# Kernel optimization log

Measured on AMD Instinct MI355X. Metric: run time of the kernel, lower is better.

The kernel has to match this reference:

```python
import jax, jax.numpy as jnp
import numpy as np

EPS_L2 = 1e-12  # torch F.normalize eps
EPS_NORM = 1e-5  # ZeroCenteredRMSNorm eps


def _linear(x, W, b):
    return x @ W.T + b


def _silu(x):
    return x * jax.nn.sigmoid(x)


def _l2norm(x):
    n = jnp.sqrt(jnp.sum(x * x, axis=-1, keepdims=True))
    return x / jnp.maximum(n, EPS_L2)


def _dwconv_causal(x, w, b):
    # x: [B,S,d]; w: [d,1,4] (torch depthwise conv weight); causal pad 3 left
    y = jax.lax.conv_general_dilated(
        x.transpose(0, 2, 1), w, window_strides=(1,), padding=[(3, 0)],
        dimension_numbers=('NCH', 'OIH', 'NCH'), feature_group_count=w.shape[0])
    return y.transpose(0, 2, 1) + b


def _zc_rmsnorm(x, weight):
    xm = x - jnp.mean(x, axis=-1, keepdims=True)
    var = jnp.mean(xm * xm, axis=-1, keepdims=True)
    return xm * jax.lax.rsqrt(var + EPS_NORM) * weight


def _gated_delta_core(q, k, v, alpha, beta):
    # q,k,v: [B,S,d]; alpha,beta: [B,S]
    B, S, d = q.shape
    S0 = jnp.zeros((B, d, d), dtype=q.dtype)

    def step(St, inp):
        qt, kt, vt, at, bt = inp  # [B,d],[B,d],[B,d],[B],[B]
        # S @ (a*(I - b k k^T)) = a*(S - b*(S k) k^T)   (rank-1 update, same math)
        Sk = jnp.einsum('bij,bj->bi', St, kt)            # [B,d]
        a = at[:, None, None]
        b = bt[:, None, None]
        Sn = a * (St - b * Sk[:, :, None] * kt[:, None, :]) + b * vt[:, :, None] * kt[:, None, :]
        ot = jnp.einsum('bij,bj->bi', Sn, qt)            # [B,d]
        return Sn, ot

    xs = (q.transpose(1, 0, 2), k.transpose(1, 0, 2), v.transpose(1, 0, 2),
          alpha.T, beta.T)
    _, outs = jax.lax.scan(step, S0, xs)  # outs: [S,B,d]
    return outs.transpose(1, 0, 2)


def setup_inputs() -> dict:
    key = jax.random.key(0)
    ks = jax.random.split(key, 16)
    B, S, d = 8, 2048, 512
    w = lambda k, shape: (jax.random.normal(k, shape, jnp.float32) * 0.02)
    return {
        'x': jax.random.normal(ks[0], (B, S, d), jnp.float32),
        'Wq': w(ks[1], (d, d)), 'bq': jnp.zeros((d,), jnp.float32),
        'Wk': w(ks[2], (d, d)), 'bk': jnp.zeros((d,), jnp.float32),
        'Wv': w(ks[3], (d, d)), 'bv': jnp.zeros((d,), jnp.float32),
        'Wa': w(ks[4], (1, d)), 'ba': jnp.zeros((1,), jnp.float32),
        'Wb': w(ks[5], (1, d)), 'bb': jnp.zeros((1,), jnp.float32),
        'cwq': w(ks[6], (d, 1, 4)), 'cbq': jnp.zeros((d,), jnp.float32),
        'cwk': w(ks[7], (d, 1, 4)), 'cbk': jnp.zeros((d,), jnp.float32),
        'cwv': w(ks[8], (d, 1, 4)), 'cbv': jnp.zeros((d,), jnp.float32),
        'norm_w': jnp.ones((d,), jnp.float32),
        'Wg': w(ks[9], (d, d)), 'bg': jnp.zeros((d,), jnp.float32),
        'Wo': w(ks[10], (d, d)), 'bo': jnp.zeros((d,), jnp.float32),
    }


def reference(x, Wq, bq, Wk, bk, Wv, bv, Wa, ba, Wb, bb,
              cwq, cbq, cwk, cbk, cwv, cbv, norm_w, Wg, bg, Wo, bo):
    q_c = _dwconv_causal(_linear(x, Wq, bq), cwq, cbq)
    k_c = _dwconv_causal(_linear(x, Wk, bk), cwk, cbk)
    v_c = _dwconv_causal(_linear(x, Wv, bv), cwv, cbv)
    q = _l2norm(_silu(q_c))
    k = _l2norm(_silu(k_c))
    v = _silu(v_c)
    alpha = jax.nn.sigmoid(_linear(x, Wa, ba))[..., 0]  # [B,S]
    beta = jax.nn.sigmoid(_linear(x, Wb, bb))[..., 0]   # [B,S]
    gdn = _gated_delta_core(q, k, v, alpha, beta)       # [B,S,d]
    gdn = _zc_rmsnorm(gdn, norm_w)
    gate = _silu(_linear(x, Wg, bg))
    return _linear(gdn * gate, Wo, bo)
```

## Files before the change

kernel.cpp:

```cpp
#include <hip/hip_runtime.h>
#include <math.h>

typedef unsigned short u16;
typedef unsigned int u32;
typedef short short8 __attribute__((ext_vector_type(8)));
typedef float f32x4 __attribute__((ext_vector_type(4)));

#define B_ 8
#define S_ 2048
#define D_ 512
#define N_ (B_ * S_)
#define ND_ ((size_t)N_ * D_)
#define CC_ 32
#define NC_ (S_ / CC_)
#define SV_ 16
#define TB_ 8

__device__ __forceinline__ u16 f2bf(float f) {
  union { float f; u32 i; } v; v.f = f;
  u32 i = v.i;
  i += 0x7FFFu + ((i >> 16) & 1u);
  return (u16)(i >> 16);
}
__device__ __forceinline__ float bf2f(u16 u) {
  union { u32 i; float f; } v; v.i = ((u32)u) << 16; return v.f;
}
__device__ __forceinline__ float sigm(float x) { return 1.0f / (1.0f + expf(-x)); }

__device__ __forceinline__ void glds16(const u16* g, u16* l) {
  __builtin_amdgcn_global_load_lds(
      (const __attribute__((address_space(1))) void*)g,
      (__attribute__((address_space(3))) void*)l, 16, 0, 0);
}

__global__ __launch_bounds__(256) void cvt_bf16(const float* __restrict__ s,
                                                u16* __restrict__ d, int n)
{
  const int i = (blockIdx.x * 256 + threadIdx.x) * 4;
  if (i < n) {
    const float4 v = *(const float4*)(s + i);
    ushort4 o;
    o.x = f2bf(v.x); o.y = f2bf(v.y); o.z = f2bf(v.z); o.w = f2bf(v.w);
    *(ushort4*)(d + i) = o;
  }
}

__global__ __launch_bounds__(256) void cvt_w5(
    const float* __restrict__ w0, const float* __restrict__ w1,
    const float* __restrict__ w2, const float* __restrict__ w3,
    const float* __restrict__ w4, u16* __restrict__ d)
{
  const int z = blockIdx.y;
  const float* s = (z == 0) ? w0 : (z == 1) ? w1 : (z == 2) ? w2 : (z == 3) ? w3 : w4;
  u16* o = d + (size_t)z * 512 * 512;
  const int i = (blockIdx.x * 256 + threadIdx.x) * 4;
  const float4 v = *(const float4*)(s + i);
  ushort4 t;
  t.x = f2bf(v.x); t.y = f2bf(v.y); t.z = f2bf(v.z); t.w = f2bf(v.w);
  *(ushort4*)(o + i) = t;
}

__device__ __forceinline__ void gemm_body(
    const u16* __restrict__ A, const u16* __restrict__ W,
    const float* __restrict__ bias, float* __restrict__ out,
    int m0, int n0, u16* As, u16* Bs)
{
  const int tid = threadIdx.x;
  const int lane = tid & 63, wave = tid >> 6;
  const int wm = (wave >> 1) * 64, wn = (wave & 1) * 64;
  const int l15 = lane & 15, quad = lane >> 4;

  const int lr = tid >> 2;
  const int ks = (tid & 3) ^ ((tid >> 3) & 3);
  u16* abase0 = As + wave * 512;
  u16* abase1 = As + 2048 + wave * 512;
  u16* bbase0 = Bs + wave * 512;
  u16* bbase1 = Bs + 2048 + wave * 512;

  f32x4 acc[4][4];
#pragma unroll
  for (int i = 0; i < 4; i++)
#pragma unroll
    for (int j = 0; j < 4; j++) acc[i][j] = (f32x4){0.f, 0.f, 0.f, 0.f};

  for (int k0 = 0; k0 < 512; k0 += 32) {
    __syncthreads();
    glds16(A + (size_t)(m0 + lr) * 512 + k0 + ks * 8, abase0);
    glds16(A + (size_t)(m0 + 64 + lr) * 512 + k0 + ks * 8, abase1);
    glds16(W + (size_t)(n0 + lr) * 512 + k0 + ks * 8, bbase0);
    glds16(W + (size_t)(n0 + 64 + lr) * 512 + k0 + ks * 8, bbase1);
    __syncthreads();
    short8 af[4], bf[4];
#pragma unroll
    for (int mt = 0; mt < 4; mt++) {
      const int row = wm + mt * 16 + l15;
      af[mt] = *(const short8*)(As + row * 32 + ((quad ^ ((row >> 1) & 3)) * 8));
    }
#pragma unroll
    for (int nt = 0; nt < 4; nt++) {
      const int row = wn + nt * 16 + l15;
      bf[nt] = *(const short8*)(Bs + row * 32 + ((quad ^ ((row >> 1) & 3)) * 8));
    }
#pragma unroll
    for (int mt = 0; mt < 4; mt++)
#pragma unroll
      for (int nt = 0; nt < 4; nt++)
        acc[mt][nt] = __builtin_amdgcn_mfma_f32_16x16x32_bf16(af[mt], bf[nt], acc[mt][nt], 0, 0, 0);
  }
#pragma unroll
  for (int mt = 0; mt < 4; mt++) {
#pragma unroll
    for (int nt = 0; nt < 4; nt++) {
      const int col = n0 + wn + nt * 16 + l15;
      const float bcol = bias[col];
#pragma unroll
      for (int r = 0; r < 4; r++) {
        const int row = m0 + wm + mt * 16 + quad * 4 + r;
        out[(size_t)row * 512 + col] = acc[mt][nt][r] + bcol;
      }
    }
  }
}

__global__ __launch_bounds__(256) void gemm_bt(
    const u16* __restrict__ A, const u16* __restrict__ W,
    const float* __restrict__ bias, float* __restrict__ out)
{
  __shared__ u16 As[128 * 32];
  __shared__ u16 Bs[128 * 32];
  gemm_body(A, W, bias, out, blockIdx.x * 128, blockIdx.y * 128, As, Bs);
}

__global__ __launch_bounds__(256) void gemm_bt4(
    const u16* __restrict__ A, const u16* __restrict__ Wbase,
    const float* __restrict__ b0, const float* __restrict__ b1,
    const float* __restrict__ b2, const float* __restrict__ b3,
    float* __restrict__ outbase)
{
  __shared__ u16 As[128 * 32];
  __shared__ u16 Bs[128 * 32];
  const int z = blockIdx.z;
  const u16* W = Wbase + (size_t)z * 512 * 512;
  const float* bias = (z == 0) ? b0 : (z == 1) ? b1 : (z == 2) ? b2 : b3;
  float* out = outbase + (size_t)z * ND_;
  gemm_body(A, W, bias, out, blockIdx.x * 128, blockIdx.y * 128, As, Bs);
}

__global__ __launch_bounds__(256) void ab_kernel(
    const float* __restrict__ x, const float* __restrict__ Wa, const float* __restrict__ ba,
    const float* __restrict__ Wb, const float* __restrict__ bb,
    float* __restrict__ alpha, float* __restrict__ beta)
{
  const int lane = threadIdx.x & 63, wave = threadIdx.x >> 6;
  const int row = blockIdx.x * 4 + wave;
  const float4 x0 = *(const float4*)(x + (size_t)row * 512 + lane * 8);
  const float4 x1 = *(const float4*)(x + (size_t)row * 512 + lane * 8 + 4);
  const float4 a0 = *(const float4*)(Wa + lane * 8);
  const float4 a1 = *(const float4*)(Wa + lane * 8 + 4);
  const float4 b0 = *(const float4*)(Wb + lane * 8);
  const float4 b1 = *(const float4*)(Wb + lane * 8 + 4);
  float da = x0.x*a0.x + x0.y*a0.y + x0.z*a0.z + x0.w*a0.w
           + x1.x*a1.x + x1.y*a1.y + x1.z*a1.z + x1.w*a1.w;
  float db = x0.x*b0.x + x0.y*b0.y + x0.z*b0.z + x0.w*b0.w
           + x1.x*b1.x + x1.y*b1.y + x1.z*b1.z + x1.w*b1.w;
#pragma unroll
  for (int m = 32; m >= 1; m >>= 1) { da += __shfl_xor(da, m, 64); db += __shfl_xor(db, m, 64); }
  if (lane == 0) {
    alpha[row] = sigm(da + ba[0]);
    beta[row]  = sigm(db + bb[0]);
  }
}

__global__ __launch_bounds__(256) void conv_act(
    const float* __restrict__ lq, const float* __restrict__ lk, const float* __restrict__ lv,
    const float* __restrict__ cwq, const float* __restrict__ cbq,
    const float* __restrict__ cwk, const float* __restrict__ cbk,
    const float* __restrict__ cwv, const float* __restrict__ cbv,
    u16* __restrict__ oq, u16* __restrict__ ok, float* __restrict__ ov)
{
  __shared__ float red[TB_][4];
  const int z = blockIdx.y;
  const int r0 = blockIdx.x * TB_;
  const int b = r0 / S_, t0 = r0 - b * S_;
  const float* lin = (z == 0) ? lq : (z == 1) ? lk : lv;
  const float* cw = (z == 0) ? cwq : (z == 1) ? cwk : cwv;
  const float* cb = (z == 0) ? cbq : (z == 1) ? cbk : cbv;
  const int tid = threadIdx.x;
  const int lane = tid & 63, wave = tid >> 6;

  float w4[2][4], bias[2];
#pragma unroll
  for (int e = 0; e < 2; e++) {
    const int ch = tid + e * 256;
    bias[e] = cb[ch];
#pragma unroll
    for (int tau = 0; tau < 4; tau++) w4[e][tau] = cw[ch * 4 + tau];
  }
  float win[2][TB_ + 3];
#pragma unroll
  for (int i = 0; i < TB_ + 3; i++) {
    const int tt = t0 - 3 + i;
#pragma unroll
    for (int e = 0; e < 2; e++)
      win[e][i] = (tt >= 0) ? lin[(size_t)(b * S_ + tt) * D_ + tid + e * 256] : 0.f;
  }
  float sv[2][TB_], ssq[TB_];
#pragma unroll
  for (int j = 0; j < TB_; j++) {
    float ss = 0.f;
#pragma unroll
    for (int e = 0; e < 2; e++) {
      float acc = bias[e];
#pragma unroll
      for (int tau = 0; tau < 4; tau++) acc = fmaf(win[e][j + tau], w4[e][tau], acc);
      const float s = acc * sigm(acc);
      sv[e][j] = s; ss = fmaf(s, s, ss);
    }
    ssq[j] = ss;
  }
  if (z < 2) {
#pragma unroll
    for (int j = 0; j < TB_; j++) {
#pragma unroll
      for (int m = 32; m >= 1; m >>= 1) ssq[j] += __shfl_xor(ssq[j], m, 64);
    }
    if (lane == 0) {
#pragma unroll
      for (int j = 0; j < TB_; j++) red[j][wave] = ssq[j];
    }
    __syncthreads();
    u16* outp = (z == 0) ? oq : ok;
#pragma unroll
    for (int j = 0; j < TB_; j++) {
      const float tot = red[j][0] + red[j][1] + red[j][2] + red[j][3];
      const float scale = 1.0f / fmaxf(sqrtf(tot), 1e-12f);
      outp[(size_t)(r0 + j) * D_ + tid] = f2bf(sv[0][j] * scale);
      outp[(size_t)(r0 + j) * D_ + tid + 256] = f2bf(sv[1][j] * scale);
    }
  } else {
#pragma unroll
    for (int j = 0; j < TB_; j++) {
      ov[(size_t)(r0 + j) * D_ + tid] = sv[0][j];
      ov[(size_t)(r0 + j) * D_ + tid + 256] = sv[1][j];
    }
  }
}

__global__ __launch_bounds__(256) void transpose_k(
    const u16* __restrict__ kh, u16* __restrict__ khT)
{
  __shared__ u16 T[64][68];
  const int b = blockIdx.z;
  const int t0 = blockIdx.x * 64;
  const int c0 = blockIdx.y * 64;
  const int tid = threadIdx.x;
  const int tr = tid >> 4;
  const int c4 = (tid & 15) * 4;
#pragma unroll
  for (int i = 0; i < 4; i++) {
    const int t = tr + i * 16;
    ushort4 v = *(const ushort4*)(kh + ((size_t)(b * S_ + t0 + t)) * 512 + c0 + c4);
    T[c4 + 0][t] = v.x; T[c4 + 1][t] = v.y; T[c4 + 2][t] = v.z; T[c4 + 3][t] = v.w;
  }
  __syncthreads();
#pragma unroll
  for (int i = 0; i < 4; i++) {
    const int ch = tr + i * 16;
    ushort4 v = *(const ushort4*)&T[ch][c4];
    *(ushort4*)(khT + ((size_t)(b * 512 + c0 + ch)) * S_ + t0 + c4) = v;
  }
}

__global__ __launch_bounds__(256) void prepass(
    const u16* __restrict__ kh, const u16* __restrict__ qh,
    float* __restrict__ vbU,
    const float* __restrict__ alpha, const float* __restrict__ beta,
    u16* __restrict__ Ag, float* __restrict__ gg, u16* __restrict__ Wc)
{
  __shared__ float KK[32][33];
  __shared__ float QK[32][33];
  __shared__ float Ml[32][33];
  __shared__ float Xs[32][33];
  __shared__ u16 Xb[32 * 40];
  __shared__ u16 VT[512 * 40];
  __shared__ float lg[32], cum[32], bet[32], gams[32];
  const int bc = blockIdx.x;
  const int b = bc >> 6, c = bc & 63;
  const int t0 = c * CC_;
  const int tid = threadIdx.x, lane = tid & 63, w = tid >> 6;
  const int l15 = lane & 15, quad = lane >> 4;
  const size_t rb = (size_t)b * S_ + t0;

  if (tid < 32) { lg[tid] = logf(alpha[b * S_ + t0 + tid]); bet[tid] = beta[b * S_ + t0 + tid]; }
  __syncthreads();
  if (tid < 32) {
    float s = 0.f;
    for (int u = 0; u <= tid; u++) s += lg[u];
    cum[tid] = s;
    gams[tid] = expf(s);
  }
  const int mi = w >> 1, ni = w & 1;
  f32x4 ck = (f32x4){0.f,0.f,0.f,0.f}, cq = ck;
#pragma unroll
  for (int kt = 0; kt < 16; kt++) {
    const int kc = kt * 32 + quad * 8;
    short8 afk = *(const short8*)(kh + (rb + mi * 16 + l15) * 512 + kc);
    short8 afq = *(const short8*)(qh + (rb + mi * 16 + l15) * 512 + kc);
    short8 bk  = *(const short8*)(kh + (rb + ni * 16 + l15) * 512 + kc);
    ck = __builtin_amdgcn_mfma_f32_16x16x32_bf16(afk, bk, ck, 0, 0, 0);
    cq = __builtin_amdgcn_mfma_f32_16x16x32_bf16(afq, bk, cq, 0, 0, 0);
  }
#pragma unroll
  for (int r = 0; r < 4; r++) {
    KK[mi * 16 + quad * 4 + r][ni * 16 + l15] = ck[r];
    QK[mi * 16 + quad * 4 + r][ni * 16 + l15] = cq[r];
  }
  __syncthreads();
  if (tid < 32) {
    gg[(size_t)bc * 64 + tid] = gams[tid];
    gg[(size_t)bc * 64 + 32 + tid] = expf(cum[31] - cum[tid]);
  }
#pragma unroll
  for (int rep = 0; rep < 4; rep++) {
    const int e = tid + rep * 256;
    const int t = e >> 5, s = e & 31;
    const float er = expf(cum[t] - cum[s]);
    Ml[t][s] = (s < t) ? bet[t] * er * KK[t][s] : 0.f;
    Ag[(size_t)bc * 1024 + t * 32 + s] = (s <= t) ? f2bf(QK[t][s] * er) : (u16)0;
  }
#pragma unroll
  for (int rep = 0; rep < 8; rep++) {
    const int e = tid + rep * 256;
    const int v = e & 511, so = e >> 9;
    short8 pk;
#pragma unroll
    for (int j = 0; j < 8; j++) {
      const int s = so * 8 + j;
      pk[j] = (short)f2bf(bet[s] * vbU[(rb + s) * 512 + v]);
    }
    *(short8*)&VT[v * 40 + so * 8] = pk;
  }
  __syncthreads();
  if (w == 0 && lane < 32) {
    const int j = lane;
    Xs[0][j] = (j == 0) ? 1.f : 0.f;
    for (int t = 1; t < 32; t++) {
      float a = (t == j) ? 1.f : 0.f;
      for (int u = 0; u < t; u++) a = fmaf(-Ml[t][u], Xs[u][j], a);
      Xs[t][j] = a;
    }
  }
  __syncthreads();
#pragma unroll
  for (int rep = 0; rep < 4; rep++) {
    const int e = tid + rep * 256;
    const int t = e >> 5, s = e & 31;
    Xb[t * 40 + s] = f2bf(Xs[t][s]);
  }
  __syncthreads();
  short8 xa[2];
  xa[0] = *(const short8*)&Xb[l15 * 40 + quad * 8];
  xa[1] = *(const short8*)&Xb[(16 + l15) * 40 + quad * 8];
#pragma unroll
  for (int ntr = 0; ntr < 8; ntr++) {
    const int nt = w * 8 + ntr;
    short8 bv = *(const short8*)&VT[(nt * 16 + l15) * 40 + quad * 8];
#pragma unroll
    for (int mt = 0; mt < 2; mt++) {
      f32x4 g = (f32x4){0.f, 0.f, 0.f, 0.f};
      g = __builtin_amdgcn_mfma_f32_16x16x32_bf16(xa[mt], bv, g, 0, 0, 0);
#pragma unroll
      for (int r = 0; r < 4; r++)
        vbU[(rb + mt * 16 + quad * 4 + r) * 512 + nt * 16 + l15] = g[r];
    }
  }
  __syncthreads();
#pragma unroll
  for (int rep = 0; rep < 8; rep++) {
    const int e = tid + rep * 256;
    const int v = e & 511, so = e >> 9;
    short8 pk;
#pragma unroll
    for (int j = 0; j < 8; j++) {
      const int s = so * 8 + j;
      pk[j] = (short)f2bf(bet[s] * gams[s] * bf2f(kh[(rb + s) * 512 + v]));
    }
    *(short8*)&VT[v * 40 + so * 8] = pk;
  }
  __syncthreads();
#pragma unroll
  for (int ntr = 0; ntr < 8; ntr++) {
    const int nt = w * 8 + ntr;
    short8 bv = *(const short8*)&VT[(nt * 16 + l15) * 40 + quad * 8];
#pragma unroll
    for (int mt = 0; mt < 2; mt++) {
      f32x4 g = (f32x4){0.f, 0.f, 0.f, 0.f};
      g = __builtin_amdgcn_mfma_f32_16x16x32_bf16(xa[mt], bv, g, 0, 0, 0);
#pragma unroll
      for (int r = 0; r < 4; r++)
        Wc[(size_t)bc * 16384 + (mt * 16 + quad * 4 + r) * 512 + nt * 16 + l15] = f2bf(g[r]);
    }
  }
}

__global__ __launch_bounds__(512) void scan_chunk(
    const u16* __restrict__ qh, const u16* __restrict__ khT,
    const u16* __restrict__ Wc, const float* __restrict__ U,
    const u16* __restrict__ Ag, const float* __restrict__ gg,
    float* __restrict__ gdn)
{
  __shared__ u16 S_A[16 * 520];
  __shared__ float P[2][2][32][16];
  __shared__ u16 Ct_T[16 * 40];
  __shared__ u16 Cr_T[16 * 40];
  __shared__ float OB[32][17];
  __shared__ float gam[32], grc[32];
  const int b = blockIdx.y;
  const int iv0 = blockIdx.x * SV_;
  const int tid = threadIdx.x, lane = tid & 63, w = tid >> 6;
  const int l15 = lane & 15, quad = lane >> 4;
  const int ttile = w & 1, mat = (w >> 1) & 1, khalf = w >> 2;
  const size_t bS = (size_t)b * S_;
  const int ct = tid >> 4, cv = tid & 15;

  f32x4 acc[4];
#pragma unroll
  for (int mt = 0; mt < 4; mt++) acc[mt] = (f32x4){0.f, 0.f, 0.f, 0.f};

  short8 nbf[8], ntk[4], nagf = {};
  float nUv = 0.f, ngam = 0.f, ngrc = 0.f;

#define SCAN_LOAD(CN) do {                                                          \
    const int t0n_ = (CN) * CC_;                                                    \
    const int bcn_ = b * 64 + (CN);                                                 \
    const u16* bsrc_ = mat ? (qh + (bS + t0n_ + ttile * 16 + l15) * 512 + khalf * 256) \
                           : (Wc + ((size_t)bcn_ * 32 + ttile * 16 + l15) * 512 + khalf * 256); \
    _Pragma("unroll")                                                               \
    for (int kt_ = 0; kt_ < 8; kt_++)                                               \
      nbf[kt_] = *(const short8*)(bsrc_ + kt_ * 32 + quad * 8);                     \
    _Pragma("unroll")                                                               \
    for (int mt_ = 0; mt_ < 4; mt_++)                                               \
      ntk[mt_] = *(const short8*)(khT + ((size_t)(b * 512 + w * 64 + mt_ * 16 + l15)) * S_ + t0n_ + quad * 8); \
    nUv = U[(bS + t0n_ + ct) * 512 + iv0 + cv];                                     \
    if (w < 2) nagf = *(const short8*)(Ag + (size_t)bcn_ * 1024 + (w * 16 + l15) * 32 + quad * 8); \
    if (tid < 32) { ngam = gg[(size_t)bcn_ * 64 + tid]; ngrc = gg[(size_t)bcn_ * 64 + 32 + tid]; } \
  } while (0)

  SCAN_LOAD(0);

#pragma unroll 1
  for (int c = 0; c < NC_; c++) {
    const int t0 = c * CC_;
    short8 bfrag[8], tk[4], agf;
#pragma unroll
    for (int kt = 0; kt < 8; kt++) bfrag[kt] = nbf[kt];
#pragma unroll
    for (int mt = 0; mt < 4; mt++) tk[mt] = ntk[mt];
    agf = nagf;
    const float Uv = nUv, gamv = ngam, grcv = ngrc;
    const int cn = (c + 1 < NC_) ? c + 1 : c;
    SCAN_LOAD(cn);
    if (tid < 32) { gam[tid] = gamv; grc[tid] = grcv; }
#pragma unroll
    for (int mt = 0; mt < 4; mt++) {
      ushort4 p;
      p.x = f2bf(acc[mt][0]); p.y = f2bf(acc[mt][1]);
      p.z = f2bf(acc[mt][2]); p.w = f2bf(acc[mt][3]);
      *(ushort4*)&S_A[l15 * 520 + w * 64 + mt * 16 + quad * 4] = p;
    }
    __syncthreads();
    f32x4 g = (f32x4){0.f, 0.f, 0.f, 0.f};
#pragma unroll
    for (int kt = 0; kt < 8; kt++) {
      short8 af = *(const short8*)&S_A[l15 * 520 + khalf * 256 + kt * 32 + quad * 8];
      g = __builtin_amdgcn_mfma_f32_16x16x32_bf16(af, bfrag[kt], g, 0, 0, 0);
    }
    *(f32x4*)&P[mat][khalf][ttile * 16 + l15][quad * 4] = g;
    __syncthreads();
    const float gCs = gam[31];
    {
      const float T1 = P[0][0][ct][cv] + P[0][1][ct][cv];
      const float T2 = P[1][0][ct][cv] + P[1][1][ct][cv];
      const float ctv = Uv - T1;
      Ct_T[cv * 40 + ct] = f2bf(ctv);
      Cr_T[cv * 40 + ct] = f2bf(ctv * grc[ct]);
      OB[ct][cv] = gam[ct] * T2;
    }
    __syncthreads();
    short8 bcf = *(const short8*)&Cr_T[l15 * 40 + quad * 8];
#pragma unroll
    for (int mt = 0; mt < 4; mt++) {
      acc[mt] = acc[mt] * gCs;
      acc[mt] = __builtin_amdgcn_mfma_f32_16x16x32_bf16(tk[mt], bcf, acc[mt], 0, 0, 0);
    }
    if (w < 2) {
      short8 ctf = *(const short8*)&Ct_T[l15 * 40 + quad * 8];
      f32x4 oo;
#pragma unroll
      for (int r = 0; r < 4; r++) oo[r] = OB[w * 16 + quad * 4 + r][l15];
      oo = __builtin_amdgcn_mfma_f32_16x16x32_bf16(agf, ctf, oo, 0, 0, 0);
#pragma unroll
      for (int r = 0; r < 4; r++)
        gdn[(bS + t0 + w * 16 + quad * 4 + r) * 512 + iv0 + l15] = oo[r];
    }
  }
#undef SCAN_LOAD
}

__global__ __launch_bounds__(256) void norm_gate(
    const float* __restrict__ gdn, const float* __restrict__ lg,
    const float* __restrict__ nw, u16* __restrict__ h)
{
  __shared__ float red[8];
  const int row = blockIdx.x, tid = threadIdx.x;
  const size_t base = (size_t)row * D_;
  const float g0 = gdn[base + tid], g1 = gdn[base + tid + 256];
  float sm = g0 + g1;
#pragma unroll
  for (int m = 32; m >= 1; m >>= 1) sm += __shfl_xor(sm, m, 64);
  if ((tid & 63) == 0) red[tid >> 6] = sm;
  __syncthreads();
  const float mean = (red[0] + red[1] + red[2] + red[3]) * (1.0f / 512.0f);
  const float x0 = g0 - mean, x1 = g1 - mean;
  float sq = x0 * x0 + x1 * x1;
#pragma unroll
  for (int m = 32; m >= 1; m >>= 1) sq += __shfl_xor(sq, m, 64);
  if ((tid & 63) == 0) red[4 + (tid >> 6)] = sq;
  __syncthreads();
  const float var = (red[4] + red[5] + red[6] + red[7]) * (1.0f / 512.0f);
  const float rst = rsqrtf(var + 1e-5f);
  const float gl0 = lg[base + tid];
  h[base + tid] = f2bf(x0 * rst * nw[tid] * (gl0 * sigm(gl0)));
  const float gl1 = lg[base + tid + 256];
  h[base + tid + 256] = f2bf(x1 * rst * nw[tid + 256] * (gl1 * sigm(gl1)));
}

extern "C" void kernel_launch(void* const* d_in, const int* in_sizes, int n_in,
                              void* d_out, int out_size, void* d_ws, size_t ws_size,
                              hipStream_t stream)
{
  const float* x   = (const float*)d_in[0];
  const float* Wq  = (const float*)d_in[1];
  const float* bq  = (const float*)d_in[2];
  const float* Wk  = (const float*)d_in[3];
  const float* bk  = (const float*)d_in[4];
  const float* Wv  = (const float*)d_in[5];
  const float* bv  = (const float*)d_in[6];
  const float* Wa  = (const float*)d_in[7];
  const float* ba  = (const float*)d_in[8];
  const float* Wb  = (const float*)d_in[9];
  const float* bb  = (const float*)d_in[10];
  const float* cwq = (const float*)d_in[11];
  const float* cbq = (const float*)d_in[12];
  const float* cwk = (const float*)d_in[13];
  const float* cbk = (const float*)d_in[14];
  const float* cwv = (const float*)d_in[15];
  const float* cbv = (const float*)d_in[16];
  const float* nw  = (const float*)d_in[17];
  const float* Wg  = (const float*)d_in[18];
  const float* bg  = (const float*)d_in[19];
  const float* Wo  = (const float*)d_in[20];
  const float* bo  = (const float*)d_in[21];

  float* ws    = (float*)d_ws;
  float* lin_q = ws;
  float* lin_k = ws + ND_;
  float* lin_v = ws + 2 * ND_;
  float* lin_g = ws + 3 * ND_;
  float* vb    = ws + 4 * ND_;
  u16*   qh    = (u16*)(ws + 5 * ND_);
  u16*   kh    = qh + ND_;
  float* alpha = ws + 6 * ND_;
  float* beta  = alpha + N_;
  u16*   xb    = (u16*)(beta + N_);
  u16*   wq_b  = xb + ND_;
  u16*   wk_b  = wq_b + 512 * 512;
  u16*   wv_b  = wk_b + 512 * 512;
  u16*   wg_b  = wv_b + 512 * 512;
  u16*   wo_b  = wg_b + 512 * 512;

  u16*   khT   = (u16*)lin_k;
  u16*   Agb   = khT + ND_;
  float* ggb   = (float*)(Agb + (size_t)512 * 1024);
  u16*   Wcb   = (u16*)lin_v;
  float* gdn   = lin_q;
  u16*   h     = (u16*)lin_v;

  const int NW = 512 * 512;
  cvt_bf16<<<(int)(ND_ / 1024), 256, 0, stream>>>(x, xb, (int)ND_);
  cvt_w5<<<dim3(NW / 1024, 5), 256, 0, stream>>>(Wq, Wk, Wv, Wg, Wo, wq_b);

  gemm_bt4<<<dim3(128, 4, 4), 256, 0, stream>>>(xb, wq_b, bq, bk, bv, bg, ws);
  ab_kernel<<<N_ / 4, 256, 0, stream>>>(x, Wa, ba, Wb, bb, alpha, beta);
  conv_act<<<dim3(N_ / TB_, 3), 256, 0, stream>>>(lin_q, lin_k, lin_v,
                                                  cwq, cbq, cwk, cbk, cwv, cbv, qh, kh, vb);
  transpose_k<<<dim3(S_ / 64, D_ / 64, B_), 256, 0, stream>>>(kh, khT);
  prepass<<<B_ * NC_, 256, 0, stream>>>(kh, qh, vb, alpha, beta, Agb, ggb, Wcb);
  scan_chunk<<<dim3(D_ / SV_, B_), 512, 0, stream>>>(qh, khT, Wcb, vb, Agb, ggb, gdn);
  norm_gate<<<N_, 256, 0, stream>>>(gdn, lin_g, nw, h);
  gemm_bt<<<dim3(128, 4), 256, 0, stream>>>(h, wo_b, bo, (float*)d_out);
}
```

Baseline: 477.7 us.

## Double chunk size to 64 in chunked delta-rule prepass and scan

Raises the chunk length of the chunked gated-delta scan from 32 to 64, which halves the number of sequential chunk iterations in scan_chunk. The prepass now builds the 64x64 triangular inverse by block inversion, solving two 32x32 diagonal blocks and combining them for the off-diagonal block, with bigger MFMA tiles over two k-steps. The scan drops its software-prefetch of the next chunk and reorganises warps so each one covers the full K=512 reduction, with no split halves to sum. Each chunk now does more work and uses more registers, and load latency is no longer hidden by prefetch.

```diff
diff --git a/kernel.cpp b/kernel.cpp
--- a/kernel.cpp
+++ b/kernel.cpp
@@ -11,7 +11,7 @@
 #define D_ 512
 #define N_ (B_ * S_)
 #define ND_ ((size_t)N_ * D_)
-#define CC_ 32
+#define CC_ 64
 #define NC_ (S_ / CC_)
 #define SV_ 16
 #define TB_ 8
@@ -277,68 +277,65 @@
     const float* __restrict__ alpha, const float* __restrict__ beta,
     u16* __restrict__ Ag, float* __restrict__ gg, u16* __restrict__ Wc)
 {
-  __shared__ float KK[32][33];
-  __shared__ float QK[32][33];
-  __shared__ float Ml[32][33];
-  __shared__ float Xs[32][33];
-  __shared__ u16 Xb[32 * 40];
-  __shared__ u16 VT[512 * 40];
-  __shared__ float lg[32], cum[32], bet[32], gams[32];
+  __shared__ __align__(16) char pool[73728];
+  float (*KK)[65]  = (float (*)[65])(pool);
+  float (*QK)[65]  = (float (*)[65])(pool + 16640);
+  float (*Ml)[65]  = (float (*)[65])(pool + 33280);
+  float (*Xs)[65]  = (float (*)[65])(pool + 49920);
+  float (*P21)[33] = (float (*)[33])(pool + 66560);
+  u16* VT = (u16*)pool;
+  __shared__ u16 Xb[64 * 72];
+  __shared__ float lg[64], cum[64], bet[64], gams[64];
   const int bc = blockIdx.x;
-  const int b = bc >> 6, c = bc & 63;
+  const int b = bc >> 5, c = bc & 31;
   const int t0 = c * CC_;
   const int tid = threadIdx.x, lane = tid & 63, w = tid >> 6;
   const int l15 = lane & 15, quad = lane >> 4;
   const size_t rb = (size_t)b * S_ + t0;
 
-  if (tid < 32) { lg[tid] = logf(alpha[b * S_ + t0 + tid]); bet[tid] = beta[b * S_ + t0 + tid]; }
-  __syncthreads();
-  if (tid < 32) {
+  if (tid < 64) { lg[tid] = logf(alpha[rb + tid]); bet[tid] = beta[rb + tid]; }
+  __syncthreads();
+  if (tid < 64) {
     float s = 0.f;
     for (int u = 0; u <= tid; u++) s += lg[u];
     cum[tid] = s;
     gams[tid] = expf(s);
   }
-  const int mi = w >> 1, ni = w & 1;
-  f32x4 ck = (f32x4){0.f,0.f,0.f,0.f}, cq = ck;
-#pragma unroll
-  for (int kt = 0; kt < 16; kt++) {
-    const int kc = kt * 32 + quad * 8;
-    short8 afk = *(const short8*)(kh + (rb + mi * 16 + l15) * 512 + kc);
-    short8 afq = *(const short8*)(qh + (rb + mi * 16 + l15) * 512 + kc);
-    short8 bk  = *(const short8*)(kh + (rb + ni * 16 + l15) * 512 + kc);
-    ck = __builtin_amdgcn_mfma_f32_16x16x32_bf16(afk, bk, ck, 0, 0, 0);
-    cq = __builtin_amdgcn_mfma_f32_16x16x32_bf16(afq, bk, cq, 0, 0, 0);
-  }
-#pragma unroll
-  for (int r = 0; r < 4; r++) {
-    KK[mi * 16 + quad * 4 + r][ni * 16 + l15] = ck[r];
-    QK[mi * 16 + quad * 4 + r][ni * 16 + l15] = cq[r];
-  }
-  __syncthreads();
-  if (tid < 32) {
-    gg[(size_t)bc * 64 + tid] = gams[tid];
-    gg[(size_t)bc * 64 + 32 + tid] = expf(cum[31] - cum[tid]);
-  }
-#pragma unroll
-  for (int rep = 0; rep < 4; rep++) {
+  __syncthreads();
+  if (tid < 64) {
+    gg[(size_t)bc * 128 + tid] = gams[tid];
+    gg[(size_t)bc * 128 + 64 + tid] = expf(cum[63] - cum[tid]);
+  }
+#pragma unroll
+  for (int rep = 0; rep < 17; rep++) {
     const int e = tid + rep * 256;
-    const int t = e >> 5, s = e & 31;
+    if (e < 64 * 65) ((float*)Xs)[e] = 0.f;
+  }
+  for (int ni = 0; ni < 4; ni++) {
+    f32x4 ck = (f32x4){0.f,0.f,0.f,0.f}, cq = ck;
+#pragma unroll
+    for (int kt = 0; kt < 16; kt++) {
+      const int kc = kt * 32 + quad * 8;
+      short8 afk = *(const short8*)(kh + (rb + w * 16 + l15) * 512 + kc);
+      short8 afq = *(const short8*)(qh + (rb + w * 16 + l15) * 512 + kc);
+      short8 bk  = *(const short8*)(kh + (rb + ni * 16 + l15) * 512 + kc);
+      ck = __builtin_amdgcn_mfma_f32_16x16x32_bf16(afk, bk, ck, 0, 0, 0);
+      cq = __builtin_amdgcn_mfma_f32_16x16x32_bf16(afq, bk, cq, 0, 0, 0);
+    }
+#pragma unroll
+    for (int r = 0; r < 4; r++) {
+      KK[w * 16 + quad * 4 + r][ni * 16 + l15] = ck[r];
+      QK[w * 16 + quad * 4 + r][ni * 16 + l15] = cq[r];
+    }
+  }
+  __syncthreads();
+#pragma unroll
+  for (int rep = 0; rep < 16; rep++) {
+    const int e = tid + rep * 256;
+    const int t = e >> 6, s = e & 63;
     const float er = expf(cum[t] - cum[s]);
     Ml[t][s] = (s < t) ? bet[t] * er * KK[t][s] : 0.f;
-    Ag[(size_t)bc * 1024 + t * 32 + s] = (s <= t) ? f2bf(QK[t][s] * er) : (u16)0;
-  }
-#pragma unroll
-  for (int rep = 0; rep < 8; rep++) {
-    const int e = tid + rep * 256;
-    const int v = e & 511, so = e >> 9;
-    short8 pk;
-#pragma unroll
-    for (int j = 0; j < 8; j++) {
-      const int s = so * 8 + j;
-      pk[j] = (short)f2bf(bet[s] * vbU[(rb + s) * 512 + v]);
-    }
-    *(short8*)&VT[v * 40 + so * 8] = pk;
+    Ag[(size_t)bc * 4096 + t * 64 + s] = (s <= t) ? f2bf(QK[t][s] * er) : (u16)0;
   }
   __syncthreads();
   if (w == 0 && lane < 32) {
@@ -350,55 +347,102 @@
       Xs[t][j] = a;
     }
   }
+  if (w == 1 && lane < 32) {
+    const int j = lane;
+    Xs[32][32 + j] = (j == 0) ? 1.f : 0.f;
+    for (int t = 1; t < 32; t++) {
+      float a = (t == j) ? 1.f : 0.f;
+      for (int u = 0; u < t; u++) a = fmaf(-Ml[32 + t][32 + u], Xs[32 + u][32 + j], a);
+      Xs[32 + t][32 + j] = a;
+    }
+  }
   __syncthreads();
 #pragma unroll
   for (int rep = 0; rep < 4; rep++) {
     const int e = tid + rep * 256;
-    const int t = e >> 5, s = e & 31;
-    Xb[t * 40 + s] = f2bf(Xs[t][s]);
-  }
-  __syncthreads();
-  short8 xa[2];
-  xa[0] = *(const short8*)&Xb[l15 * 40 + quad * 8];
-  xa[1] = *(const short8*)&Xb[(16 + l15) * 40 + quad * 8];
-#pragma unroll
-  for (int ntr = 0; ntr < 8; ntr++) {
-    const int nt = w * 8 + ntr;
-    short8 bv = *(const short8*)&VT[(nt * 16 + l15) * 40 + quad * 8];
-#pragma unroll
-    for (int mt = 0; mt < 2; mt++) {
-      f32x4 g = (f32x4){0.f, 0.f, 0.f, 0.f};
-      g = __builtin_amdgcn_mfma_f32_16x16x32_bf16(xa[mt], bv, g, 0, 0, 0);
-#pragma unroll
-      for (int r = 0; r < 4; r++)
-        vbU[(rb + mt * 16 + quad * 4 + r) * 512 + nt * 16 + l15] = g[r];
-    }
-  }
-  __syncthreads();
-#pragma unroll
-  for (int rep = 0; rep < 8; rep++) {
+    const int i = e >> 5, j = e & 31;
+    float a = 0.f;
+    for (int u = 0; u < 32; u++) a = fmaf(Ml[32 + i][u], Xs[u][j], a);
+    P21[i][j] = a;
+  }
+  __syncthreads();
+#pragma unroll
+  for (int rep = 0; rep < 4; rep++) {
+    const int e = tid + rep * 256;
+    const int i = e >> 5, j = e & 31;
+    float a = 0.f;
+    for (int u = 0; u < 32; u++) a = fmaf(Xs[32 + i][32 + u], P21[u][j], a);
+    Xs[32 + i][j] = -a;
+  }
+  __syncthreads();
+#pragma unroll
+  for (int rep = 0; rep < 16; rep++) {
+    const int e = tid + rep * 256;
+    const int t = e >> 6, s = e & 63;
+    Xb[t * 72 + s] = f2bf(Xs[t][s]);
+  }
+  __syncthreads();
+#pragma unroll
+  for (int rep = 0; rep < 16; rep++) {
     const int e = tid + rep * 256;
     const int v = e & 511, so = e >> 9;
     short8 pk;
 #pragma unroll
     for (int j = 0; j < 8; j++) {
       const int s = so * 8 + j;
-      pk[j] = (short)f2bf(bet[s] * gams[s] * bf2f(kh[(rb + s) * 512 + v]));
-    }
-    *(short8*)&VT[v * 40 + so * 8] = pk;
-  }
-  __syncthreads();
+      pk[j] = (short)f2bf(bet[s] * vbU[(rb + s) * 512 + v]);
+    }
+    *(short8*)&VT[v * 72 + so * 8] = pk;
+  }
+  __syncthreads();
+  short8 xa[4][2];
+#pragma unroll
+  for (int mt = 0; mt < 4; mt++)
+#pragma unroll
+    for (int ks = 0; ks < 2; ks++)
+      xa[mt][ks] = *(const short8*)&Xb[(mt * 16 + l15) * 72 + ks * 32 + quad * 8];
 #pragma unroll
   for (int ntr = 0; ntr < 8; ntr++) {
     const int nt = w * 8 + ntr;
-    short8 bv = *(const short8*)&VT[(nt * 16 + l15) * 40 + quad * 8];
-#pragma unroll
-    for (int mt = 0; mt < 2; mt++) {
+    short8 bv0 = *(const short8*)&VT[(nt * 16 + l15) * 72 + quad * 8];
+    short8 bv1 = *(const short8*)&VT[(nt * 16 + l15) * 72 + 32 + quad * 8];
+#pragma unroll
+    for (int mt = 0; mt < 4; mt++) {
       f32x4 g = (f32x4){0.f, 0.f, 0.f, 0.f};
-      g = __builtin_amdgcn_mfma_f32_16x16x32_bf16(xa[mt], bv, g, 0, 0, 0);
+      g = __builtin_amdgcn_mfma_f32_16x16x32_bf16(xa[mt][0], bv0, g, 0, 0, 0);
+      g = __builtin_amdgcn_mfma_f32_16x16x32_bf16(xa[mt][1], bv1, g, 0, 0, 0);
 #pragma unroll
       for (int r = 0; r < 4; r++)
-        Wc[(size_t)bc * 16384 + (mt * 16 + quad * 4 + r) * 512 + nt * 16 + l15] = f2bf(g[r]);
+        vbU[(rb + mt * 16 + quad * 4 + r) * 512 + nt * 16 + l15] = g[r];
+    }
+  }
+  __syncthreads();
+#pragma unroll
+  for (int rep = 0; rep < 16; rep++) {
+    const int e = tid + rep * 256;
+    const int v = e & 511, so = e >> 9;
+    short8 pk;
+#pragma unroll
+    for (int j = 0; j < 8; j++) {
+      const int s = so * 8 + j;
+      pk[j] = (short)f2bf(bet[s] * gams[s] * bf2f(kh[(rb + s) * 512 + v]));
+    }
+    *(short8*)&VT[v * 72 + so * 8] = pk;
+  }
+  __syncthreads();
+#pragma unroll
+  for (int ntr = 0; ntr < 8; ntr++) {
+    const int nt = w * 8 + ntr;
+    short8 bv0 = *(const short8*)&VT[(nt * 16 + l15) * 72 + quad * 8];
+    short8 bv1 = *(const short8*)&VT[(nt * 16 + l15) * 72 + 32 + quad * 8];
+#pragma unroll
+    for (int mt = 0; mt < 4; mt++) {
+      f32x4 g = (f32x4){0.f, 0.f, 0.f, 0.f};
+      g = __builtin_amdgcn_mfma_f32_16x16x32_bf16(xa[mt][0], bv0, g, 0, 0, 0);
+      g = __builtin_amdgcn_mfma_f32_16x16x32_bf16(xa[mt][1], bv1, g, 0, 0, 0);
+#pragma unroll
+      for (int r = 0; r < 4; r++)
+        Wc[((size_t)bc * 64 + mt * 16 + quad * 4 + r) * 512 + nt * 16 + l15] = f2bf(g[r]);
     }
   }
 }
@@ -410,57 +454,50 @@
     float* __restrict__ gdn)
 {
   __shared__ u16 S_A[16 * 520];
-  __shared__ float P[2][2][32][16];
-  __shared__ u16 Ct_T[16 * 40];
-  __shared__ u16 Cr_T[16 * 40];
-  __shared__ float OB[32][17];
-  __shared__ float gam[32], grc[32];
+  __shared__ float P[2][64][20];
+  __shared__ u16 Ct_T[16 * 72];
+  __shared__ u16 Cr_T[16 * 72];
+  __shared__ float OB[64][17];
+  __shared__ float gam[64], grc[64];
   const int b = blockIdx.y;
   const int iv0 = blockIdx.x * SV_;
   const int tid = threadIdx.x, lane = tid & 63, w = tid >> 6;
   const int l15 = lane & 15, quad = lane >> 4;
-  const int ttile = w & 1, mat = (w >> 1) & 1, khalf = w >> 2;
+  const int mat = w & 1, ttile = w >> 1;
   const size_t bS = (size_t)b * S_;
-  const int ct = tid >> 4, cv = tid & 15;
+  const int ct = tid >> 3, cvp = (tid & 7) * 2;
 
   f32x4 acc[4];
 #pragma unroll
   for (int mt = 0; mt < 4; mt++) acc[mt] = (f32x4){0.f, 0.f, 0.f, 0.f};
-
-  short8 nbf[8], ntk[4], nagf = {};
-  float nUv = 0.f, ngam = 0.f, ngrc = 0.f;
-
-#define SCAN_LOAD(CN) do {                                                          \
-    const int t0n_ = (CN) * CC_;                                                    \
-    const int bcn_ = b * 64 + (CN);                                                 \
-    const u16* bsrc_ = mat ? (qh + (bS + t0n_ + ttile * 16 + l15) * 512 + khalf * 256) \
-                           : (Wc + ((size_t)bcn_ * 32 + ttile * 16 + l15) * 512 + khalf * 256); \
-    _Pragma("unroll")                                                               \
-    for (int kt_ = 0; kt_ < 8; kt_++)                                               \
-      nbf[kt_] = *(const short8*)(bsrc_ + kt_ * 32 + quad * 8);                     \
-    _Pragma("unroll")                                                               \
-    for (int mt_ = 0; mt_ < 4; mt_++)                                               \
-      ntk[mt_] = *(const short8*)(khT + ((size_t)(b * 512 + w * 64 + mt_ * 16 + l15)) * S_ + t0n_ + quad * 8); \
-    nUv = U[(bS + t0n_ + ct) * 512 + iv0 + cv];                                     \
-    if (w < 2) nagf = *(const short8*)(Ag + (size_t)bcn_ * 1024 + (w * 16 + l15) * 32 + quad * 8); \
-    if (tid < 32) { ngam = gg[(size_t)bcn_ * 64 + tid]; ngrc = gg[(size_t)bcn_ * 64 + 32 + tid]; } \
-  } while (0)
-
-  SCAN_LOAD(0);
 
 #pragma unroll 1
   for (int c = 0; c < NC_; c++) {
     const int t0 = c * CC_;
-    short8 bfrag[8], tk[4], agf;
-#pragma unroll
-    for (int kt = 0; kt < 8; kt++) bfrag[kt] = nbf[kt];
-#pragma unroll
-    for (int mt = 0; mt < 4; mt++) tk[mt] = ntk[mt];
-    agf = nagf;
-    const float Uv = nUv, gamv = ngam, grcv = ngrc;
-    const int cn = (c + 1 < NC_) ? c + 1 : c;
-    SCAN_LOAD(cn);
-    if (tid < 32) { gam[tid] = gamv; grc[tid] = grcv; }
+    const int bc = b * NC_ + c;
+    short8 bfrag[16];
+    const u16* bsrc = mat ? (qh + (bS + t0 + ttile * 16 + l15) * 512)
+                          : (Wc + ((size_t)bc * 64 + ttile * 16 + l15) * 512);
+#pragma unroll
+    for (int kt = 0; kt < 16; kt++)
+      bfrag[kt] = *(const short8*)(bsrc + kt * 32 + quad * 8);
+    short8 tk[4][2];
+#pragma unroll
+    for (int mt = 0; mt < 4; mt++)
+#pragma unroll
+      for (int ks = 0; ks < 2; ks++)
+        tk[mt][ks] = *(const short8*)(khT + ((size_t)(b * 512 + w * 64 + mt * 16 + l15)) * S_ + t0 + ks * 32 + quad * 8);
+    float Uv[2];
+#pragma unroll
+    for (int e = 0; e < 2; e++)
+      Uv[e] = U[(bS + t0 + ct) * 512 + iv0 + cvp + e];
+    short8 agf[2];
+    if (w < 4) {
+#pragma unroll
+      for (int ks = 0; ks < 2; ks++)
+        agf[ks] = *(const short8*)(Ag + (size_t)bc * 4096 + (w * 16 + l15) * 64 + ks * 32 + quad * 8);
+    }
+    if (tid < 64) { gam[tid] = gg[(size_t)bc * 128 + tid]; grc[tid] = gg[(size_t)bc * 128 + 64 + tid]; }
 #pragma unroll
     for (int mt = 0; mt < 4; mt++) {
       ushort4 p;
@@ -469,42 +506,52 @@
       *(ushort4*)&S_A[l15 * 520 + w * 64 + mt * 16 + quad * 4] = p;
     }
     __syncthreads();
-    f32x4 g = (f32x4){0.f, 0.f, 0.f, 0.f};
-#pragma unroll
-    for (int kt = 0; kt < 8; kt++) {
-      short8 af = *(const short8*)&S_A[l15 * 520 + khalf * 256 + kt * 32 + quad * 8];
-      g = __builtin_amdgcn_mfma_f32_16x16x32_bf16(af, bfrag[kt], g, 0, 0, 0);
-    }
-    *(f32x4*)&P[mat][khalf][ttile * 16 + l15][quad * 4] = g;
+    f32x4 g0 = (f32x4){0.f, 0.f, 0.f, 0.f}, g1 = g0;
+#pragma unroll
+    for (int kt = 0; kt < 16; kt += 2) {
+      short8 af0 = *(const short8*)&S_A[l15 * 520 + kt * 32 + quad * 8];
+      short8 af1 = *(const short8*)&S_A[l15 * 520 + (kt + 1) * 32 + quad * 8];
+      g0 = __builtin_amdgcn_mfma_f32_16x16x32_bf16(af0, bfrag[kt], g0, 0, 0, 0);
+      g1 = __builtin_amdgcn_mfma_f32_16x16x32_bf16(af1, bfrag[kt + 1], g1, 0, 0, 0);
+    }
+    {
+      f32x4 g = g0 + g1;
+      *(f32x4*)&P[mat][ttile * 16 + l15][quad * 4] = g;
+    }
     __syncthreads();
-    const float gCs = gam[31];
-    {
-      const float T1 = P[0][0][ct][cv] + P[0][1][ct][cv];
-      const float T2 = P[1][0][ct][cv] + P[1][1][ct][cv];
-      const float ctv = Uv - T1;
-      Ct_T[cv * 40 + ct] = f2bf(ctv);
-      Cr_T[cv * 40 + ct] = f2bf(ctv * grc[ct]);
+    const float gCs = gam[63];
+#pragma unroll
+    for (int e = 0; e < 2; e++) {
+      const int cv = cvp + e;
+      const float T1 = P[0][ct][cv];
+      const float T2 = P[1][ct][cv];
+      const float ctv = Uv[e] - T1;
+      Ct_T[cv * 72 + ct] = f2bf(ctv);
+      Cr_T[cv * 72 + ct] = f2bf(ctv * grc[ct]);
       OB[ct][cv] = gam[ct] * T2;
     }
     __syncthreads();
-    short8 bcf = *(const short8*)&Cr_T[l15 * 40 + quad * 8];
+    short8 bcf0 = *(const short8*)&Cr_T[l15 * 72 + quad * 8];
+    short8 bcf1 = *(const short8*)&Cr_T[l15 * 72 + 32 + quad * 8];
 #pragma unroll
     for (int mt = 0; mt < 4; mt++) {
       acc[mt] = acc[mt] * gCs;
-      acc[mt] = __builtin_amdgcn_mfma_f32_16x16x32_bf16(tk[mt], bcf, acc[mt], 0, 0, 0);
-    }
-    if (w < 2) {
-      short8 ctf = *(const short8*)&Ct_T[l15 * 40 + quad * 8];
+      acc[mt] = __builtin_amdgcn_mfma_f32_16x16x32_bf16(tk[mt][0], bcf0, acc[mt], 0, 0, 0);
+      acc[mt] = __builtin_amdgcn_mfma_f32_16x16x32_bf16(tk[mt][1], bcf1, acc[mt], 0, 0, 0);
+    }
+    if (w < 4) {
+      short8 ctf0 = *(const short8*)&Ct_T[l15 * 72 + quad * 8];
+      short8 ctf1 = *(const short8*)&Ct_T[l15 * 72 + 32 + quad * 8];
       f32x4 oo;
 #pragma unroll
       for (int r = 0; r < 4; r++) oo[r] = OB[w * 16 + quad * 4 + r][l15];
-      oo = __builtin_amdgcn_mfma_f32_16x16x32_bf16(agf, ctf, oo, 0, 0, 0);
+      oo = __builtin_amdgcn_mfma_f32_16x16x32_bf16(agf[0], ctf0, oo, 0, 0, 0);
+      oo = __builtin_amdgcn_mfma_f32_16x16x32_bf16(agf[1], ctf1, oo, 0, 0, 0);
 #pragma unroll
       for (int r = 0; r < 4; r++)
         gdn[(bS + t0 + w * 16 + quad * 4 + r) * 512 + iv0 + l15] = oo[r];
     }
   }
-#undef SCAN_LOAD
 }
 
 __global__ __launch_bounds__(256) void norm_gate(
@@ -581,7 +628,7 @@
 
   u16*   khT   = (u16*)lin_k;
   u16*   Agb   = khT + ND_;
-  float* ggb   = (float*)(Agb + (size_t)512 * 1024);
+  float* ggb   = (float*)(Agb + (size_t)256 * 4096);
   u16*   Wcb   = (u16*)lin_v;
   float* gdn   = lin_q;
   u16*   h     = (u16*)lin_v;
```

Measured after the change: 514.1 us. 1.08x slower.
